# Performance work log

Measured on AMD Instinct MI355X. Metric: run time of the kernel, lower is better.

Reference implementation:

```python
import jax, jax.numpy as jnp
import numpy as np

NUM_TOKENS = 16384
HIDDEN = 2048
NUM_EXPERTS = 64
TOP_K = 2


def setup_inputs() -> dict:
    key = jax.random.key(0)
    kx, kw = jax.random.split(key)
    x = jax.random.normal(kx, (NUM_TOKENS, HIDDEN), dtype=jnp.float32)
    # nn.Linear weight is (num_experts, hidden); store transposed for x @ W
    W_gate = jax.random.normal(kw, (HIDDEN, NUM_EXPERTS), dtype=jnp.float32) * (1.0 / np.sqrt(HIDDEN))
    return {"x": x, "W_gate": W_gate}


def reference(x, W_gate):
    # gate matmul + softmax over experts
    logits = jnp.einsum("th,he->te", x, W_gate)          # (T, E)
    probs = jax.nn.softmax(logits, axis=-1)
    # top-k selection and renormalization
    top_k_weights, top_k_indices = jax.lax.top_k(probs, TOP_K)  # (T, k), (T, k)
    top_k_weights = top_k_weights / (jnp.sum(top_k_weights, axis=-1, keepdims=True) + 1e-9)
    # Switch-style load-balancing aux loss using top-1 assignments
    num_tokens = x.shape[0]
    top1 = top_k_indices[:, 0]
    tokens_per_expert = jnp.zeros((NUM_EXPERTS,), dtype=probs.dtype).at[top1].add(1.0)
    f = tokens_per_expert / num_tokens                    # fraction of tokens per expert
    P = jnp.mean(probs, axis=0)                           # mean router prob per expert
    aux_loss = NUM_EXPERTS * jnp.sum(f * P)
    return (top_k_weights, top_k_indices, aux_loss)
```

## Files before the change

### kernel.cpp

```cpp
#include <hip/hip_runtime.h>
#include <math.h>

#define NUM_TOKENS 16384
#define HIDDEN 2048
#define NUM_EXPERTS 64

#define IDX_OFF 32768
#define AUX_OFF 65536

#define TPW 8
#define WPB 4
#define TPB (TPW * WPB)
#define NBLK (NUM_TOKENS / TPB)
#define BK 128

__device__ __forceinline__ void gll16(const float* g, float* l) {
    __builtin_amdgcn_global_load_lds(
        (const __attribute__((address_space(1))) unsigned int*)g,
        (__attribute__((address_space(3))) unsigned int*)l, 16, 0, 0);
}

__global__ __launch_bounds__(256, 2) void router_kernel(
    const float* __restrict__ x, const float* __restrict__ Wg,
    float* __restrict__ out, float* __restrict__ ws)
{
    __shared__ float lds_w[2][BK][NUM_EXPERTS];

    const int tid = threadIdx.x;
    const int w   = tid >> 6;
    const int lane = tid & 63;
    const int ph  = lane >> 4;
    const int eq  = lane & 15;
    const int tok0 = blockIdx.x * TPB + w * TPW;

    float C[TPW][4];
    #pragma unroll
    for (int t = 0; t < TPW; ++t)
        #pragma unroll
        for (int j = 0; j < 4; ++j) C[t][j] = 0.f;

    const float* xrow = x + (size_t)tok0 * HIDDEN + ph * 4;

    #define STAGE(buf, kbn) { \
        const float* gsrc = Wg + (size_t)(kbn) * NUM_EXPERTS; \
        float* ldst = &lds_w[buf][0][0]; \
        _Pragma("unroll") \
        for (int i = 0; i < 8; ++i) \
            gll16(gsrc + i * 1024 + tid * 4, ldst + i * 1024 + tid * 4); \
    }

    STAGE(0, 0);
    float4 xA[TPW], xB[TPW];
    #pragma unroll
    for (int t = 0; t < TPW; ++t)
        xA[t] = *reinterpret_cast<const float4*>(xrow + (size_t)t * HIDDEN);
    __syncthreads();

    for (int kb = 0; kb < HIDDEN; kb += BK) {
        const int bsel = (kb >> 7) & 1;
        if (kb + BK < HIDDEN) STAGE(bsel ^ 1, kb + BK);

        #pragma unroll
        for (int ks8 = 0; ks8 < 8; ++ks8) {
            float4* curp = (ks8 & 1) ? xB : xA;
            float4* nxtp = (ks8 & 1) ? xA : xB;

            {
                int kn = kb + ks8 * 16 + 16;
                if (kn >= HIDDEN) kn = 0;
                #pragma unroll
                for (int t = 0; t < TPW; ++t)
                    nxtp[t] = *reinterpret_cast<const float4*>(
                        xrow + (size_t)t * HIDDEN + kn);
            }

            float4 wv[4];
            #pragma unroll
            for (int jj = 0; jj < 4; ++jj)
                wv[jj] = *reinterpret_cast<const float4*>(
                    &lds_w[bsel][ks8 * 16 + ph * 4 + jj][eq * 4]);

            #pragma unroll
            for (int t = 0; t < TPW; ++t) {
                const float xs[4] = {curp[t].x, curp[t].y, curp[t].z, curp[t].w};
                #pragma unroll
                for (int jj = 0; jj < 4; ++jj) {
                    C[t][0] = fmaf(xs[jj], wv[jj].x, C[t][0]);
                    C[t][1] = fmaf(xs[jj], wv[jj].y, C[t][1]);
                    C[t][2] = fmaf(xs[jj], wv[jj].z, C[t][2]);
                    C[t][3] = fmaf(xs[jj], wv[jj].w, C[t][3]);
                }
            }
        }
        __syncthreads();
    }

    #pragma unroll
    for (int t = 0; t < TPW; ++t)
        #pragma unroll
        for (int j = 0; j < 4; ++j) {
            float v = C[t][j];
            v += __shfl_xor(v, 16);
            v += __shfl_xor(v, 32);
            C[t][j] = v;
        }

    float* logits = &lds_w[0][0][0];
    float* sP = logits + TPB * 68;
    float* sC = sP + WPB * 64;
    if (ph == 0) {
        #pragma unroll
        for (int t = 0; t < TPW; ++t) {
            float4 v; v.x = C[t][0]; v.y = C[t][1]; v.z = C[t][2]; v.w = C[t][3];
            *reinterpret_cast<float4*>(&logits[(w * TPW + t) * 68 + eq * 4]) = v;
        }
    }
    __syncthreads();

    float accP = 0.f, accC = 0.f;
    #pragma unroll
    for (int t = 0; t < TPW; ++t) {
        const float l = logits[(w * TPW + t) * 68 + lane];
        float m = l;
        #pragma unroll
        for (int off = 32; off >= 1; off >>= 1) m = fmaxf(m, __shfl_xor(m, off));
        const float p = expf(l - m);
        float Z = p;
        #pragma unroll
        for (int off = 32; off >= 1; off >>= 1) Z += __shfl_xor(Z, off);
        const float prob = p / Z;

        float v1 = prob; int i1 = lane;
        #pragma unroll
        for (int off = 32; off >= 1; off >>= 1) {
            const float ov = __shfl_xor(v1, off);
            const int   oi = __shfl_xor(i1, off);
            if (ov > v1 || (ov == v1 && oi < i1)) { v1 = ov; i1 = oi; }
        }
        float v2 = (lane == i1) ? -1.f : prob; int i2 = lane;
        #pragma unroll
        for (int off = 32; off >= 1; off >>= 1) {
            const float ov = __shfl_xor(v2, off);
            const int   oi = __shfl_xor(i2, off);
            if (ov > v2 || (ov == v2 && oi < i2)) { v2 = ov; i2 = oi; }
        }

        accP += prob;
        accC += (lane == i1) ? 1.f : 0.f;

        if (lane == 0) {
            const float s = v1 + v2 + 1e-9f;
            const size_t o = (size_t)(tok0 + t) * 2;
            float2 wo; wo.x = v1 / s; wo.y = v2 / s;
            *reinterpret_cast<float2*>(&out[o]) = wo;
            float2 io; io.x = (float)i1; io.y = (float)i2;
            *reinterpret_cast<float2*>(&out[IDX_OFF + o]) = io;
        }
    }

    sP[w * 64 + lane] = accP;
    sC[w * 64 + lane] = accC;
    __syncthreads();
    if (tid < 64) {
        const float sp = sP[tid] + sP[64 + tid] + sP[128 + tid] + sP[192 + tid];
        const float sc = sC[tid] + sC[64 + tid] + sC[128 + tid] + sC[192 + tid];
        ws[(size_t)blockIdx.x * 128 + tid]      = sp;
        ws[(size_t)blockIdx.x * 128 + 64 + tid] = sc;
    }
}

__global__ __launch_bounds__(64) void finalize_kernel(
    const float* __restrict__ ws, float* __restrict__ out)
{
    const int e = threadIdx.x;
    float sp = 0.f, sc = 0.f;
    for (int b = 0; b < NBLK; ++b) {
        sp += ws[(size_t)b * 128 + e];
        sc += ws[(size_t)b * 128 + 64 + e];
    }
    float val = (sc * (1.0f / NUM_TOKENS)) * (sp * (1.0f / NUM_TOKENS));
    #pragma unroll
    for (int off = 32; off >= 1; off >>= 1) val += __shfl_xor(val, off);
    if (e == 0) out[AUX_OFF] = (float)NUM_EXPERTS * val;
}

extern "C" void kernel_launch(void* const* d_in, const int* in_sizes, int n_in,
                              void* d_out, int out_size, void* d_ws, size_t ws_size,
                              hipStream_t stream) {
    const float* x  = (const float*)d_in[0];
    const float* Wg = (const float*)d_in[1];
    float* out = (float*)d_out;
    float* ws  = (float*)d_ws;

    router_kernel<<<NBLK, 256, 0, stream>>>(x, Wg, out, ws);
    finalize_kernel<<<1, 64, 0, stream>>>(ws, out);
}
```

Measured before the change: 112.3 us.

## Split hidden dimension across two warp groups and use packed FMA

Each block now runs 512 threads in two groups, and each group accumulates half of the hidden dimension for the same 32 tokens. The partial logits are combined through LDS before softmax and top-k, which group 0 handles. The K tile shrinks to 32 per group, and the accumulators use 2-wide vector FMA so the compiler can emit packed FP32 ops. The aim is more waves per CU to hide latency on x loads and higher FMA throughput, at the cost of an extra LDS reduction and idle threads during the epilogue.

```diff
diff --git a/kernel.cpp b/kernel.cpp
--- a/kernel.cpp
+++ b/kernel.cpp
@@ -9,10 +9,12 @@
 #define AUX_OFF 65536
 
 #define TPW 8
-#define WPB 4
-#define TPB (TPW * WPB)
+#define TPB 32
 #define NBLK (NUM_TOKENS / TPB)
-#define BK 128
+#define KG (HIDDEN / 2)
+#define BK 32
+
+typedef float v2f __attribute__((ext_vector_type(2)));
 
 __device__ __forceinline__ void gll16(const float* g, float* l) {
     __builtin_amdgcn_global_load_lds(
@@ -20,147 +22,174 @@
         (__attribute__((address_space(3))) unsigned int*)l, 16, 0, 0);
 }
 
-__global__ __launch_bounds__(256, 2) void router_kernel(
+__global__ __launch_bounds__(512, 4) void router_kernel(
     const float* __restrict__ x, const float* __restrict__ Wg,
     float* __restrict__ out, float* __restrict__ ws)
 {
-    __shared__ float lds_w[2][BK][NUM_EXPERTS];
-
-    const int tid = threadIdx.x;
-    const int w   = tid >> 6;
+    __shared__ float lds_w[2][2][BK][NUM_EXPERTS];
+
+    const int tid  = threadIdx.x;
+    const int g    = tid >> 8;
+    const int wi   = (tid >> 6) & 3;
+    const int gtid = tid & 255;
     const int lane = tid & 63;
-    const int ph  = lane >> 4;
-    const int eq  = lane & 15;
-    const int tok0 = blockIdx.x * TPB + w * TPW;
-
-    float C[TPW][4];
-    #pragma unroll
-    for (int t = 0; t < TPW; ++t)
-        #pragma unroll
-        for (int j = 0; j < 4; ++j) C[t][j] = 0.f;
-
-    const float* xrow = x + (size_t)tok0 * HIDDEN + ph * 4;
-
-    #define STAGE(buf, kbn) { \
-        const float* gsrc = Wg + (size_t)(kbn) * NUM_EXPERTS; \
-        float* ldst = &lds_w[buf][0][0]; \
+    const int ph   = lane >> 4;
+    const int eq   = lane & 15;
+    const int tok0 = blockIdx.x * TPB + wi * TPW;
+
+    v2f C2[TPW][2];
+    #pragma unroll
+    for (int t = 0; t < TPW; ++t) { C2[t][0] = (v2f)(0.f); C2[t][1] = (v2f)(0.f); }
+
+    const float* xrow = x + (size_t)tok0 * HIDDEN + g * KG + ph * 4;
+
+    #define STAGE(buf, kbg) { \
+        const float* gsrc = Wg + (size_t)(kbg) * NUM_EXPERTS; \
+        float* ldst = &lds_w[g][buf][0][0]; \
         _Pragma("unroll") \
-        for (int i = 0; i < 8; ++i) \
-            gll16(gsrc + i * 1024 + tid * 4, ldst + i * 1024 + tid * 4); \
-    }
-
-    STAGE(0, 0);
+        for (int i = 0; i < 2; ++i) \
+            gll16(gsrc + (i * 256 + gtid) * 4, ldst + (i * 256 + gtid) * 4); \
+    }
+
+    STAGE(0, g * KG);
     float4 xA[TPW], xB[TPW];
     #pragma unroll
     for (int t = 0; t < TPW; ++t)
         xA[t] = *reinterpret_cast<const float4*>(xrow + (size_t)t * HIDDEN);
     __syncthreads();
 
-    for (int kb = 0; kb < HIDDEN; kb += BK) {
-        const int bsel = (kb >> 7) & 1;
-        if (kb + BK < HIDDEN) STAGE(bsel ^ 1, kb + BK);
-
-        #pragma unroll
-        for (int ks8 = 0; ks8 < 8; ++ks8) {
-            float4* curp = (ks8 & 1) ? xB : xA;
-            float4* nxtp = (ks8 & 1) ? xA : xB;
+    for (int kb = 0; kb < KG; kb += BK) {
+        const int bsel = (kb >> 5) & 1;
+        if (kb + BK < KG) STAGE(bsel ^ 1, g * KG + kb + BK);
+
+        #pragma unroll
+        for (int ks = 0; ks < 2; ++ks) {
+            float4* curp = ks ? xB : xA;
+            float4* nxtp = ks ? xA : xB;
 
             {
-                int kn = kb + ks8 * 16 + 16;
-                if (kn >= HIDDEN) kn = 0;
+                int kn = kb + ks * 16 + 16;
+                if (kn >= KG) kn = 0;
                 #pragma unroll
                 for (int t = 0; t < TPW; ++t)
                     nxtp[t] = *reinterpret_cast<const float4*>(
                         xrow + (size_t)t * HIDDEN + kn);
             }
 
-            float4 wv[4];
-            #pragma unroll
-            for (int jj = 0; jj < 4; ++jj)
-                wv[jj] = *reinterpret_cast<const float4*>(
-                    &lds_w[bsel][ks8 * 16 + ph * 4 + jj][eq * 4]);
+            v2f wv[4][2];
+            #pragma unroll
+            for (int jj = 0; jj < 4; ++jj) {
+                const float4 v = *reinterpret_cast<const float4*>(
+                    &lds_w[g][bsel][ks * 16 + ph * 4 + jj][eq * 4]);
+                wv[jj][0] = (v2f){v.x, v.y};
+                wv[jj][1] = (v2f){v.z, v.w};
+            }
 
             #pragma unroll
             for (int t = 0; t < TPW; ++t) {
                 const float xs[4] = {curp[t].x, curp[t].y, curp[t].z, curp[t].w};
                 #pragma unroll
                 for (int jj = 0; jj < 4; ++jj) {
-                    C[t][0] = fmaf(xs[jj], wv[jj].x, C[t][0]);
-                    C[t][1] = fmaf(xs[jj], wv[jj].y, C[t][1]);
-                    C[t][2] = fmaf(xs[jj], wv[jj].z, C[t][2]);
-                    C[t][3] = fmaf(xs[jj], wv[jj].w, C[t][3]);
+                    const v2f xsp = (v2f){xs[jj], xs[jj]};
+                    C2[t][0] = __builtin_elementwise_fma(xsp, wv[jj][0], C2[t][0]);
+                    C2[t][1] = __builtin_elementwise_fma(xsp, wv[jj][1], C2[t][1]);
                 }
             }
         }
         __syncthreads();
     }
 
-    #pragma unroll
-    for (int t = 0; t < TPW; ++t)
+    float Cf[TPW][4];
+    #pragma unroll
+    for (int t = 0; t < TPW; ++t) {
+        Cf[t][0] = C2[t][0].x; Cf[t][1] = C2[t][0].y;
+        Cf[t][2] = C2[t][1].x; Cf[t][3] = C2[t][1].y;
         #pragma unroll
         for (int j = 0; j < 4; ++j) {
-            float v = C[t][j];
+            float v = Cf[t][j];
             v += __shfl_xor(v, 16);
             v += __shfl_xor(v, 32);
-            C[t][j] = v;
-        }
-
-    float* logits = &lds_w[0][0][0];
-    float* sP = logits + TPB * 68;
-    float* sC = sP + WPB * 64;
-    if (ph == 0) {
+            Cf[t][j] = v;
+        }
+    }
+
+    float* lgB = &lds_w[0][0][0][0];
+    float* lgA = lgB + TPB * 68;
+    float* sP  = lgA + TPB * 68;
+    float* sC  = sP + 4 * 64;
+
+    if (g == 1 && ph == 0) {
         #pragma unroll
         for (int t = 0; t < TPW; ++t) {
-            float4 v; v.x = C[t][0]; v.y = C[t][1]; v.z = C[t][2]; v.w = C[t][3];
-            *reinterpret_cast<float4*>(&logits[(w * TPW + t) * 68 + eq * 4]) = v;
-        }
-    }
-    __syncthreads();
-
-    float accP = 0.f, accC = 0.f;
-    #pragma unroll
-    for (int t = 0; t < TPW; ++t) {
-        const float l = logits[(w * TPW + t) * 68 + lane];
-        float m = l;
-        #pragma unroll
-        for (int off = 32; off >= 1; off >>= 1) m = fmaxf(m, __shfl_xor(m, off));
-        const float p = expf(l - m);
-        float Z = p;
-        #pragma unroll
-        for (int off = 32; off >= 1; off >>= 1) Z += __shfl_xor(Z, off);
-        const float prob = p / Z;
-
-        float v1 = prob; int i1 = lane;
-        #pragma unroll
-        for (int off = 32; off >= 1; off >>= 1) {
-            const float ov = __shfl_xor(v1, off);
-            const int   oi = __shfl_xor(i1, off);
-            if (ov > v1 || (ov == v1 && oi < i1)) { v1 = ov; i1 = oi; }
-        }
-        float v2 = (lane == i1) ? -1.f : prob; int i2 = lane;
-        #pragma unroll
-        for (int off = 32; off >= 1; off >>= 1) {
-            const float ov = __shfl_xor(v2, off);
-            const int   oi = __shfl_xor(i2, off);
-            if (ov > v2 || (ov == v2 && oi < i2)) { v2 = ov; i2 = oi; }
-        }
-
-        accP += prob;
-        accC += (lane == i1) ? 1.f : 0.f;
-
-        if (lane == 0) {
-            const float s = v1 + v2 + 1e-9f;
-            const size_t o = (size_t)(tok0 + t) * 2;
-            float2 wo; wo.x = v1 / s; wo.y = v2 / s;
-            *reinterpret_cast<float2*>(&out[o]) = wo;
-            float2 io; io.x = (float)i1; io.y = (float)i2;
-            *reinterpret_cast<float2*>(&out[IDX_OFF + o]) = io;
-        }
-    }
-
-    sP[w * 64 + lane] = accP;
-    sC[w * 64 + lane] = accC;
-    __syncthreads();
+            float4 v; v.x = Cf[t][0]; v.y = Cf[t][1]; v.z = Cf[t][2]; v.w = Cf[t][3];
+            *reinterpret_cast<float4*>(&lgB[(wi * TPW + t) * 68 + eq * 4]) = v;
+        }
+    }
+    __syncthreads();
+
+    if (g == 0) {
+        #pragma unroll
+        for (int t = 0; t < TPW; ++t) {
+            const float4 v = *reinterpret_cast<const float4*>(
+                &lgB[(wi * TPW + t) * 68 + eq * 4]);
+            Cf[t][0] += v.x; Cf[t][1] += v.y; Cf[t][2] += v.z; Cf[t][3] += v.w;
+        }
+        if (ph == 0) {
+            #pragma unroll
+            for (int t = 0; t < TPW; ++t) {
+                float4 v; v.x = Cf[t][0]; v.y = Cf[t][1]; v.z = Cf[t][2]; v.w = Cf[t][3];
+                *reinterpret_cast<float4*>(&lgA[(wi * TPW + t) * 68 + eq * 4]) = v;
+            }
+        }
+    }
+    __syncthreads();
+
+    if (g == 0) {
+        float accP = 0.f, accC = 0.f;
+        #pragma unroll
+        for (int t = 0; t < TPW; ++t) {
+            const float l = lgA[(wi * TPW + t) * 68 + lane];
+            float m = l;
+            #pragma unroll
+            for (int off = 32; off >= 1; off >>= 1) m = fmaxf(m, __shfl_xor(m, off));
+            const float p = expf(l - m);
+            float Z = p;
+            #pragma unroll
+            for (int off = 32; off >= 1; off >>= 1) Z += __shfl_xor(Z, off);
+            const float prob = p / Z;
+
+            float v1 = prob; int i1 = lane;
+            #pragma unroll
+            for (int off = 32; off >= 1; off >>= 1) {
+                const float ov = __shfl_xor(v1, off);
+                const int   oi = __shfl_xor(i1, off);
+                if (ov > v1 || (ov == v1 && oi < i1)) { v1 = ov; i1 = oi; }
+            }
+            float v2 = (lane == i1) ? -1.f : prob; int i2 = lane;
+            #pragma unroll
+            for (int off = 32; off >= 1; off >>= 1) {
+                const float ov = __shfl_xor(v2, off);
+                const int   oi = __shfl_xor(i2, off);
+                if (ov > v2 || (ov == v2 && oi < i2)) { v2 = ov; i2 = oi; }
+            }
+
+            accP += prob;
+            accC += (lane == i1) ? 1.f : 0.f;
+
+            if (lane == 0) {
+                const float s = v1 + v2 + 1e-9f;
+                const size_t o = (size_t)(tok0 + t) * 2;
+                float2 wo; wo.x = v1 / s; wo.y = v2 / s;
+                *reinterpret_cast<float2*>(&out[o]) = wo;
+                float2 io; io.x = (float)i1; io.y = (float)i2;
+                *reinterpret_cast<float2*>(&out[IDX_OFF + o]) = io;
+            }
+        }
+        sP[wi * 64 + lane] = accP;
+        sC[wi * 64 + lane] = accC;
+    }
+    __syncthreads();
+
     if (tid < 64) {
         const float sp = sP[tid] + sP[64 + tid] + sP[128 + tid] + sP[192 + tid];
         const float sc = sC[tid] + sC[64 + tid] + sC[128 + tid] + sC[192 + tid];
@@ -192,6 +221,6 @@
     float* out = (float*)d_out;
     float* ws  = (float*)d_ws;
 
-    router_kernel<<<NBLK, 256, 0, stream>>>(x, Wg, out, ws);
+    router_kernel<<<NBLK, 512, 0, stream>>>(x, Wg, out, ws);
     finalize_kernel<<<1, 64, 0, stream>>>(ws, out);
 }
```

Result: faster. 109.0 us (-3.0%).

## Split hidden dimension across waves with cross-wave reduction, read weights directly

Applied to the files above, without the earlier changes.

Each block now handles 8 tokens, with its 8 waves each covering a K-slice of the hidden dimension, and reduces partial logits through LDS before wave 0 runs softmax/top-k. The LDS double-buffered weight staging is removed in favor of direct global loads of W, and the FMAs use packed 2-wide vector FMA. The finalize kernel spreads the per-block reduction across 4 waves. This raises parallelism and drops LDS staging, but re-reads W from cache per block and serialises the epilogue on one wave.

```diff
diff --git a/kernel.cpp b/kernel.cpp
--- a/kernel.cpp
+++ b/kernel.cpp
@@ -8,180 +8,155 @@
 #define IDX_OFF 32768
 #define AUX_OFF 65536
 
-#define TPW 8
-#define WPB 4
-#define TPB (TPW * WPB)
+#define TPB 8
 #define NBLK (NUM_TOKENS / TPB)
-#define BK 128
+#define KSL (HIDDEN / 8)
+#define NCK (KSL / 16)
 
-__device__ __forceinline__ void gll16(const float* g, float* l) {
-    __builtin_amdgcn_global_load_lds(
-        (const __attribute__((address_space(1))) unsigned int*)g,
-        (__attribute__((address_space(3))) unsigned int*)l, 16, 0, 0);
-}
+typedef float v2f __attribute__((ext_vector_type(2)));
 
-__global__ __launch_bounds__(256, 2) void router_kernel(
+__global__ __launch_bounds__(512, 4) void router_kernel(
     const float* __restrict__ x, const float* __restrict__ Wg,
     float* __restrict__ out, float* __restrict__ ws)
 {
-    __shared__ float lds_w[2][BK][NUM_EXPERTS];
+    __shared__ float red[8][TPB][68];
 
-    const int tid = threadIdx.x;
-    const int w   = tid >> 6;
+    const int tid  = threadIdx.x;
+    const int w    = __builtin_amdgcn_readfirstlane(tid >> 6);
     const int lane = tid & 63;
-    const int ph  = lane >> 4;
-    const int eq  = lane & 15;
-    const int tok0 = blockIdx.x * TPB + w * TPW;
+    const int ph   = lane >> 4;
+    const int eq   = lane & 15;
+    const int tok0 = blockIdx.x * TPB;
+    const int k0   = w * KSL;
 
-    float C[TPW][4];
+    v2f C2[TPB][2];
     #pragma unroll
-    for (int t = 0; t < TPW; ++t)
+    for (int t = 0; t < TPB; ++t) { C2[t][0] = (v2f)(0.f); C2[t][1] = (v2f)(0.f); }
+
+    const float* xb = x  + (size_t)tok0 * HIDDEN + k0 + ph * 4;
+    const float* wb = Wg + (size_t)k0 * NUM_EXPERTS + eq * 4;
+
+    for (int ck = 0; ck < NCK; ++ck) {
+        float4 xv[TPB];
         #pragma unroll
-        for (int j = 0; j < 4; ++j) C[t][j] = 0.f;
-
-    const float* xrow = x + (size_t)tok0 * HIDDEN + ph * 4;
-
-    #define STAGE(buf, kbn) { \
-        const float* gsrc = Wg + (size_t)(kbn) * NUM_EXPERTS; \
-        float* ldst = &lds_w[buf][0][0]; \
-        _Pragma("unroll") \
-        for (int i = 0; i < 8; ++i) \
-            gll16(gsrc + i * 1024 + tid * 4, ldst + i * 1024 + tid * 4); \
+        for (int t = 0; t < TPB; ++t)
+            xv[t] = *reinterpret_cast<const float4*>(
+                xb + (size_t)t * HIDDEN + ck * 16);
+        float4 wv[4];
+        #pragma unroll
+        for (int jj = 0; jj < 4; ++jj)
+            wv[jj] = *reinterpret_cast<const float4*>(
+                wb + (size_t)(ck * 16 + ph * 4 + jj) * NUM_EXPERTS);
+        #pragma unroll
+        for (int t = 0; t < TPB; ++t) {
+            const float xs[4] = {xv[t].x, xv[t].y, xv[t].z, xv[t].w};
+            #pragma unroll
+            for (int jj = 0; jj < 4; ++jj) {
+                const v2f a = (v2f){xs[jj], xs[jj]};
+                C2[t][0] = __builtin_elementwise_fma(a, (v2f){wv[jj].x, wv[jj].y}, C2[t][0]);
+                C2[t][1] = __builtin_elementwise_fma(a, (v2f){wv[jj].z, wv[jj].w}, C2[t][1]);
+            }
+        }
     }
 
-    STAGE(0, 0);
-    float4 xA[TPW], xB[TPW];
+    float Cf[TPB][4];
     #pragma unroll
-    for (int t = 0; t < TPW; ++t)
-        xA[t] = *reinterpret_cast<const float4*>(xrow + (size_t)t * HIDDEN);
-    __syncthreads();
-
-    for (int kb = 0; kb < HIDDEN; kb += BK) {
-        const int bsel = (kb >> 7) & 1;
-        if (kb + BK < HIDDEN) STAGE(bsel ^ 1, kb + BK);
-
+    for (int t = 0; t < TPB; ++t) {
+        Cf[t][0] = C2[t][0].x; Cf[t][1] = C2[t][0].y;
+        Cf[t][2] = C2[t][1].x; Cf[t][3] = C2[t][1].y;
         #pragma unroll
-        for (int ks8 = 0; ks8 < 8; ++ks8) {
-            float4* curp = (ks8 & 1) ? xB : xA;
-            float4* nxtp = (ks8 & 1) ? xA : xB;
-
-            {
-                int kn = kb + ks8 * 16 + 16;
-                if (kn >= HIDDEN) kn = 0;
-                #pragma unroll
-                for (int t = 0; t < TPW; ++t)
-                    nxtp[t] = *reinterpret_cast<const float4*>(
-                        xrow + (size_t)t * HIDDEN + kn);
-            }
-
-            float4 wv[4];
-            #pragma unroll
-            for (int jj = 0; jj < 4; ++jj)
-                wv[jj] = *reinterpret_cast<const float4*>(
-                    &lds_w[bsel][ks8 * 16 + ph * 4 + jj][eq * 4]);
-
-            #pragma unroll
-            for (int t = 0; t < TPW; ++t) {
-                const float xs[4] = {curp[t].x, curp[t].y, curp[t].z, curp[t].w};
-                #pragma unroll
-                for (int jj = 0; jj < 4; ++jj) {
-                    C[t][0] = fmaf(xs[jj], wv[jj].x, C[t][0]);
-                    C[t][1] = fmaf(xs[jj], wv[jj].y, C[t][1]);
-                    C[t][2] = fmaf(xs[jj], wv[jj].z, C[t][2]);
-                    C[t][3] = fmaf(xs[jj], wv[jj].w, C[t][3]);
-                }
-            }
+        for (int j = 0; j < 4; ++j) {
+            float v = Cf[t][j];
+            v += __shfl_xor(v, 16);
+            v += __shfl_xor(v, 32);
+            Cf[t][j] = v;
         }
-        __syncthreads();
     }
 
-    #pragma unroll
-    for (int t = 0; t < TPW; ++t)
-        #pragma unroll
-        for (int j = 0; j < 4; ++j) {
-            float v = C[t][j];
-            v += __shfl_xor(v, 16);
-            v += __shfl_xor(v, 32);
-            C[t][j] = v;
-        }
-
-    float* logits = &lds_w[0][0][0];
-    float* sP = logits + TPB * 68;
-    float* sC = sP + WPB * 64;
     if (ph == 0) {
         #pragma unroll
-        for (int t = 0; t < TPW; ++t) {
-            float4 v; v.x = C[t][0]; v.y = C[t][1]; v.z = C[t][2]; v.w = C[t][3];
-            *reinterpret_cast<float4*>(&logits[(w * TPW + t) * 68 + eq * 4]) = v;
+        for (int t = 0; t < TPB; ++t) {
+            float4 v; v.x = Cf[t][0]; v.y = Cf[t][1]; v.z = Cf[t][2]; v.w = Cf[t][3];
+            *reinterpret_cast<float4*>(&red[w][t][eq * 4]) = v;
         }
     }
     __syncthreads();
 
-    float accP = 0.f, accC = 0.f;
-    #pragma unroll
-    for (int t = 0; t < TPW; ++t) {
-        const float l = logits[(w * TPW + t) * 68 + lane];
-        float m = l;
+    if (w == 0) {
+        float accP = 0.f, accC = 0.f;
         #pragma unroll
-        for (int off = 32; off >= 1; off >>= 1) m = fmaxf(m, __shfl_xor(m, off));
-        const float p = expf(l - m);
-        float Z = p;
-        #pragma unroll
-        for (int off = 32; off >= 1; off >>= 1) Z += __shfl_xor(Z, off);
-        const float prob = p / Z;
+        for (int t = 0; t < TPB; ++t) {
+            float l = 0.f;
+            #pragma unroll
+            for (int s = 0; s < 8; ++s) l += red[s][t][lane];
 
-        float v1 = prob; int i1 = lane;
-        #pragma unroll
-        for (int off = 32; off >= 1; off >>= 1) {
-            const float ov = __shfl_xor(v1, off);
-            const int   oi = __shfl_xor(i1, off);
-            if (ov > v1 || (ov == v1 && oi < i1)) { v1 = ov; i1 = oi; }
+            float m = l;
+            #pragma unroll
+            for (int off = 32; off >= 1; off >>= 1) m = fmaxf(m, __shfl_xor(m, off));
+            const float p = expf(l - m);
+            float Z = p;
+            #pragma unroll
+            for (int off = 32; off >= 1; off >>= 1) Z += __shfl_xor(Z, off);
+            const float prob = p / Z;
+
+            float v1 = prob; int i1 = lane;
+            #pragma unroll
+            for (int off = 32; off >= 1; off >>= 1) {
+                const float ov = __shfl_xor(v1, off);
+                const int   oi = __shfl_xor(i1, off);
+                if (ov > v1 || (ov == v1 && oi < i1)) { v1 = ov; i1 = oi; }
+            }
+            float v2 = (lane == i1) ? -1.f : prob; int i2 = lane;
+            #pragma unroll
+            for (int off = 32; off >= 1; off >>= 1) {
+                const float ov = __shfl_xor(v2, off);
+                const int   oi = __shfl_xor(i2, off);
+                if (ov > v2 || (ov == v2 && oi < i2)) { v2 = ov; i2 = oi; }
+            }
+
+            accP += prob;
+            accC += (lane == i1) ? 1.f : 0.f;
+
+            if (lane == 0) {
+                const float s = v1 + v2 + 1e-9f;
+                const size_t o = (size_t)(tok0 + t) * 2;
+                float2 wo; wo.x = v1 / s; wo.y = v2 / s;
+                *reinterpret_cast<float2*>(&out[o]) = wo;
+                float2 io; io.x = (float)i1; io.y = (float)i2;
+                *reinterpret_cast<float2*>(&out[IDX_OFF + o]) = io;
+            }
         }
-        float v2 = (lane == i1) ? -1.f : prob; int i2 = lane;
-        #pragma unroll
-        for (int off = 32; off >= 1; off >>= 1) {
-            const float ov = __shfl_xor(v2, off);
-            const int   oi = __shfl_xor(i2, off);
-            if (ov > v2 || (ov == v2 && oi < i2)) { v2 = ov; i2 = oi; }
-        }
-
-        accP += prob;
-        accC += (lane == i1) ? 1.f : 0.f;
-
-        if (lane == 0) {
-            const float s = v1 + v2 + 1e-9f;
-            const size_t o = (size_t)(tok0 + t) * 2;
-            float2 wo; wo.x = v1 / s; wo.y = v2 / s;
-            *reinterpret_cast<float2*>(&out[o]) = wo;
-            float2 io; io.x = (float)i1; io.y = (float)i2;
-            *reinterpret_cast<float2*>(&out[IDX_OFF + o]) = io;
-        }
-    }
-
-    sP[w * 64 + lane] = accP;
-    sC[w * 64 + lane] = accC;
-    __syncthreads();
-    if (tid < 64) {
-        const float sp = sP[tid] + sP[64 + tid] + sP[128 + tid] + sP[192 + tid];
-        const float sc = sC[tid] + sC[64 + tid] + sC[128 + tid] + sC[192 + tid];
-        ws[(size_t)blockIdx.x * 128 + tid]      = sp;
-        ws[(size_t)blockIdx.x * 128 + 64 + tid] = sc;
+        ws[(size_t)blockIdx.x * 128 + lane]      = accP;
+        ws[(size_t)blockIdx.x * 128 + 64 + lane] = accC;
     }
 }
 
-__global__ __launch_bounds__(64) void finalize_kernel(
+__global__ __launch_bounds__(256) void finalize_kernel(
     const float* __restrict__ ws, float* __restrict__ out)
 {
-    const int e = threadIdx.x;
+    __shared__ float sbuf[2][4][64];
+    const int tid = threadIdx.x;
+    const int q   = tid >> 6;
+    const int e   = tid & 63;
+
     float sp = 0.f, sc = 0.f;
-    for (int b = 0; b < NBLK; ++b) {
+    #pragma unroll 4
+    for (int b = q; b < NBLK; b += 4) {
         sp += ws[(size_t)b * 128 + e];
         sc += ws[(size_t)b * 128 + 64 + e];
     }
-    float val = (sc * (1.0f / NUM_TOKENS)) * (sp * (1.0f / NUM_TOKENS));
-    #pragma unroll
-    for (int off = 32; off >= 1; off >>= 1) val += __shfl_xor(val, off);
-    if (e == 0) out[AUX_OFF] = (float)NUM_EXPERTS * val;
+    sbuf[0][q][e] = sp;
+    sbuf[1][q][e] = sc;
+    __syncthreads();
+
+    if (tid < 64) {
+        const float tsp = sbuf[0][0][e] + sbuf[0][1][e] + sbuf[0][2][e] + sbuf[0][3][e];
+        const float tsc = sbuf[1][0][e] + sbuf[1][1][e] + sbuf[1][2][e] + sbuf[1][3][e];
+        float val = (tsc * (1.0f / NUM_TOKENS)) * (tsp * (1.0f / NUM_TOKENS));
+        #pragma unroll
+        for (int off = 32; off >= 1; off >>= 1) val += __shfl_xor(val, off);
+        if (e == 0) out[AUX_OFF] = (float)NUM_EXPERTS * val;
+    }
 }
 
 extern "C" void kernel_launch(void* const* d_in, const int* in_sizes, int n_in,
@@ -192,6 +167,6 @@
     float* out = (float*)d_out;
     float* ws  = (float*)d_ws;
 
-    router_kernel<<<NBLK, 256, 0, stream>>>(x, Wg, out, ws);
-    finalize_kernel<<<1, 64, 0, stream>>>(ws, out);
+    router_kernel<<<NBLK, 512, 0, stream>>>(x, Wg, out, ws);
+    finalize_kernel<<<1, 256, 0, stream>>>(ws, out);
 }
```

After: 173.3 us. +54.3%, slower.
